# Performance work log

Hardware: AMD Instinct MI355X
Metric: run time of the kernel (lower is better)

Reference implementation:

```python
import jax, jax.numpy as jnp
import numpy as np

N_NODES = 50000
N_EDGES = 800000
N_FEAT = 128
HIDDEN = 64
EMBED = 300
N_CLASSES = 10
N_GRAPHS = 500
LEAKY_SLOPE = 0.01  # torch F.leaky_relu default


def gcn_conv(x, W, b, src, dst, n_nodes):
    # PyG GCNConv: h = x @ W; add self-loops; norm = deg^{-1/2}[src] * deg^{-1/2}[dst]
    h = x @ W  # [N, H]
    deg = jax.ops.segment_sum(jnp.ones_like(dst, dtype=h.dtype), dst, num_segments=n_nodes) + 1.0  # +1 self-loop
    dis = jax.lax.rsqrt(deg)  # deg^{-1/2}, deg >= 1 so finite
    norm = dis[src] * dis[dst]  # [E]
    agg = jax.ops.segment_sum(h[src] * norm[:, None], dst, num_segments=n_nodes)
    agg = agg + h * (dis * dis)[:, None]  # self-loop contribution
    return agg + b


def segment_softmax(s, seg, num_segments):
    # s: [N, 1]; softmax over nodes within each graph
    m = jax.ops.segment_max(s, seg, num_segments=num_segments)
    e = jnp.exp(s - m[seg])
    z = jax.ops.segment_sum(e, seg, num_segments=num_segments)
    return e / z[seg]


def setup_inputs() -> dict:
    key = jax.random.key(0)
    ks = jax.random.split(key, 16)

    def glorot(k, shape):
        fan_in, fan_out = shape[0], shape[1]
        lim = np.sqrt(6.0 / (fan_in + fan_out)).astype(np.float32)
        return jax.random.uniform(k, shape, jnp.float32, -lim, lim)

    x = jax.random.normal(ks[0], (N_NODES, N_FEAT), jnp.float32)
    edge_index = jax.random.randint(ks[1], (2, N_EDGES), 0, N_NODES, dtype=jnp.int64)
    batch = jnp.sort(jax.random.randint(ks[2], (N_NODES,), 0, N_GRAPHS, dtype=jnp.int64))
    return {
        "x": x,
        "edge_index": edge_index,
        "batch": batch,
        "W1": glorot(ks[3], (N_FEAT, HIDDEN)),
        "b1": jnp.zeros((HIDDEN,), jnp.float32),
        "W2": glorot(ks[4], (HIDDEN, HIDDEN)),
        "b2": jnp.zeros((HIDDEN,), jnp.float32),
        "att_w": glorot(ks[5], (HIDDEN, 1)),
        "att_b": jnp.zeros((1,), jnp.float32),
        "proj_w": glorot(ks[6], (HIDDEN, EMBED)),
        "proj_b": jnp.zeros((EMBED,), jnp.float32),
        "cls_w1": glorot(ks[7], (EMBED, 128)),
        "cls_b1": jnp.zeros((128,), jnp.float32),
        "cls_w2": glorot(ks[8], (128, N_CLASSES)),
        "cls_b2": jnp.zeros((N_CLASSES,), jnp.float32),
    }


def reference(x, edge_index, batch, W1, b1, W2, b2, att_w, att_b, proj_w, proj_b, cls_w1, cls_b1, cls_w2, cls_b2):
    src, dst = edge_index[0], edge_index[1]
    n_nodes = x.shape[0]
    h = jax.nn.relu(gcn_conv(x, W1, b1, src, dst, n_nodes))
    # dropout is identity in eval mode
    h = jax.nn.relu(gcn_conv(h, W2, b2, src, dst, n_nodes))  # [N, H]
    att = jax.nn.leaky_relu(h @ att_w + att_b, negative_slope=LEAKY_SLOPE)  # [N, 1]
    att = segment_softmax(att, batch, N_GRAPHS)
    g = jax.ops.segment_sum(att * h, batch, num_segments=N_GRAPHS)  # [G, H]
    g = g @ proj_w + proj_b  # [G, EMBED]
    out = jax.nn.relu(g @ cls_w1 + cls_b1) @ cls_w2 + cls_b2  # [G, num_classes]
    return out
```

## Files before the change

### kernel.cpp

```cpp
#include <hip/hip_runtime.h>
#include <hip/hip_fp16.h>
#include <math.h>

#define N_NODES   50000
#define N_EDGES   800000
#define N_FEAT    128
#define HIDDEN    64
#define EMBED     300
#define N_CLASSES 10
#define N_GRAPHS  500
#define LEAKY     0.01f
#define SCAN_BLOCKS ((N_NODES + 255) / 256)
#define G1_ROWS   32

typedef __attribute__((ext_vector_type(4))) _Float16 half4f;

__device__ __forceinline__ float pk_w(unsigned p) {
    return __half2float(__ushort_as_half((unsigned short)(p >> 16)));
}

__global__ void k_zero(int* deg, int* gs, int* ge) {
    int i = blockIdx.x * 256 + threadIdx.x;
    if (i < N_NODES) deg[i] = 0;
    if (i < N_GRAPHS) { gs[i] = 0; ge[i] = 0; }
}

__global__ void k_deg_rank(const int* __restrict__ dst, int* deg, int* rank) {
    int e = blockIdx.x * 256 + threadIdx.x;
    if (e < N_EDGES) rank[e] = atomicAdd(&deg[dst[e]], 1);
}

__global__ __launch_bounds__(256) void k_scan1(const int* __restrict__ deg, int* row_start,
                                               int* partials, float* dis) {
    __shared__ int wsum[4];
    int i = blockIdx.x * 256 + threadIdx.x;
    int v = (i < N_NODES) ? deg[i] : 0;
    int lane = threadIdx.x & 63, wid = threadIdx.x >> 6;
    int s = v;
    #pragma unroll
    for (int off = 1; off < 64; off <<= 1) {
        int t = __shfl_up(s, off, 64);
        if (lane >= off) s += t;
    }
    if (lane == 63) wsum[wid] = s;
    __syncthreads();
    int woff = 0;
    for (int w = 0; w < wid; ++w) woff += wsum[w];
    if (i < N_NODES) {
        row_start[i] = woff + s - v;
        dis[i] = rsqrtf((float)(deg[i] + 1));
    }
    if (threadIdx.x == 255) partials[blockIdx.x] = woff + s;
}

__global__ __launch_bounds__(256) void k_scan2(int* partials) {
    __shared__ int wsum[4];
    int v = (threadIdx.x < SCAN_BLOCKS) ? partials[threadIdx.x] : 0;
    int lane = threadIdx.x & 63, wid = threadIdx.x >> 6;
    int s = v;
    #pragma unroll
    for (int off = 1; off < 64; off <<= 1) {
        int t = __shfl_up(s, off, 64);
        if (lane >= off) s += t;
    }
    if (lane == 63) wsum[wid] = s;
    __syncthreads();
    int woff = 0;
    for (int w = 0; w < wid; ++w) woff += wsum[w];
    if (threadIdx.x < SCAN_BLOCKS) partials[threadIdx.x] = woff + s - v;
}

__global__ void k_scan3(int* row_start, const int* __restrict__ partials) {
    int i = blockIdx.x * 256 + threadIdx.x;
    if (i < N_NODES) row_start[i] += partials[blockIdx.x];
    if (i == 0) row_start[N_NODES] = N_EDGES;
}

__global__ void k_fill(const int* __restrict__ src, const int* __restrict__ dst,
                       const int* __restrict__ rank, const int* __restrict__ row_start,
                       const float* __restrict__ dis, unsigned* __restrict__ pk) {
    int e = blockIdx.x * 256 + threadIdx.x;
    if (e < N_EDGES) {
        int s = src[e], d = dst[e];
        float w = dis[s] * dis[d];
        unsigned short wh = __half_as_ushort(__float2half(w));
        pk[row_start[d] + rank[e]] = (unsigned)s | ((unsigned)wh << 16);
    }
}

__global__ __launch_bounds__(256) void k_gemm1(const float* __restrict__ x,
                                               const float* __restrict__ W,
                                               __half* __restrict__ h) {
    __shared__ float sW[N_FEAT * HIDDEN];
    __shared__ float sx[G1_ROWS * N_FEAT];
    {
        const float4* W4 = (const float4*)W;
        float4* sW4 = (float4*)sW;
        #pragma unroll
        for (int i = 0; i < N_FEAT * HIDDEN / 4 / 256; ++i)
            sW4[i * 256 + threadIdx.x] = W4[i * 256 + threadIdx.x];

        int base = blockIdx.x * G1_ROWS;
        const float4* x4 = (const float4*)(x + (size_t)base * N_FEAT);
        float4* sx4 = (float4*)sx;
        int lim = (N_NODES - base) * (N_FEAT / 4);
        #pragma unroll
        for (int i = 0; i < G1_ROWS * N_FEAT / 4 / 256; ++i) {
            int idx = i * 256 + threadIdx.x;
            sx4[idx] = (idx < lim) ? x4[idx] : make_float4(0.f, 0.f, 0.f, 0.f);
        }
    }
    __syncthreads();

    int f = threadIdx.x & 63, wid = threadIdx.x >> 6;
    float acc[8];
    #pragma unroll
    for (int u = 0; u < 8; ++u) acc[u] = 0.0f;

    const float4* sx4 = (const float4*)sx;
    #pragma unroll 4
    for (int k4 = 0; k4 < N_FEAT / 4; ++k4) {
        float w0 = sW[(k4 * 4 + 0) * HIDDEN + f];
        float w1 = sW[(k4 * 4 + 1) * HIDDEN + f];
        float w2 = sW[(k4 * 4 + 2) * HIDDEN + f];
        float w3 = sW[(k4 * 4 + 3) * HIDDEN + f];
        #pragma unroll
        for (int u = 0; u < 8; ++u) {
            float4 xv = sx4[(wid * 8 + u) * (N_FEAT / 4) + k4];
            acc[u] = fmaf(xv.x, w0, fmaf(xv.y, w1, fmaf(xv.z, w2, fmaf(xv.w, w3, acc[u]))));
        }
    }
    int base = blockIdx.x * G1_ROWS;
    #pragma unroll
    for (int u = 0; u < 8; ++u) {
        int n = base + wid * 8 + u;
        if (n < N_NODES) h[(size_t)n * HIDDEN + f] = __float2half(acc[u]);
    }
}

__device__ __forceinline__ void gather4pk(const __half* __restrict__ h,
                                          const unsigned* __restrict__ pk,
                                          int s, int e, int lane, int g4, int q,
                                          float4& acc) {
    for (int cs = s; cs < e; cs += 64) {
        unsigned pkv = (cs + lane < e) ? pk[cs + lane] : 0u;
        int avail = e - cs; if (avail > 64) avail = 64;
        int iters = (avail + 3) >> 2;
        #pragma unroll 2
        for (int t = 0; t < iters; ++t) {
            unsigned p = __shfl(pkv, t * 4 + g4, 64);
            float w = pk_w(p);
            half4f hv = *(const half4f*)(h + ((size_t)(p & 0xFFFFu)) * HIDDEN + (q << 2));
            acc.x = fmaf(w, (float)hv.x, acc.x);
            acc.y = fmaf(w, (float)hv.y, acc.y);
            acc.z = fmaf(w, (float)hv.z, acc.z);
            acc.w = fmaf(w, (float)hv.w, acc.w);
        }
    }
}

__device__ __forceinline__ void xreduce(float4& a) {
    a.x += __shfl_xor(a.x, 16, 64); a.y += __shfl_xor(a.y, 16, 64);
    a.z += __shfl_xor(a.z, 16, 64); a.w += __shfl_xor(a.w, 16, 64);
    a.x += __shfl_xor(a.x, 32, 64); a.y += __shfl_xor(a.y, 32, 64);
    a.z += __shfl_xor(a.z, 32, 64); a.w += __shfl_xor(a.w, 32, 64);
}

__global__ __launch_bounds__(256) void k_gg(const __half* __restrict__ h1,
                                            const unsigned* __restrict__ pk,
                                            const int* __restrict__ row_start,
                                            const float* __restrict__ dis,
                                            const float* __restrict__ b1,
                                            const float* __restrict__ W2,
                                            __half* __restrict__ h2) {
    __shared__ float sW[HIDDEN * HIDDEN];
    __shared__ float sa[16 * HIDDEN];
    {
        const float4* W4 = (const float4*)W2;
        float4* sW4 = (float4*)sW;
        #pragma unroll
        for (int i = 0; i < 4; ++i)
            sW4[i * 256 + threadIdx.x] = W4[i * 256 + threadIdx.x];
    }

    int tid = threadIdx.x, wid = tid >> 6, lane = tid & 63;
    int g4 = lane >> 4, q = lane & 15;
    int base = blockIdx.x * 16 + wid * 4;
    #pragma unroll
    for (int i = 0; i < 4; ++i) {
        int node = base + i;
        int s = row_start[node], e = row_start[node + 1];
        float4 acc = {0.f, 0.f, 0.f, 0.f};
        gather4pk(h1, pk, s, e, lane, g4, q, acc);
        xreduce(acc);
        float dv = dis[node], dd = dv * dv;
        half4f sv = *(const half4f*)(h1 + (size_t)node * HIDDEN + (q << 2));
        float4 bv = *(const float4*)(b1 + (q << 2));
        float4 r;
        r.x = fmaxf(fmaf((float)sv.x, dd, bv.x) + acc.x, 0.f);
        r.y = fmaxf(fmaf((float)sv.y, dd, bv.y) + acc.y, 0.f);
        r.z = fmaxf(fmaf((float)sv.z, dd, bv.z) + acc.z, 0.f);
        r.w = fmaxf(fmaf((float)sv.w, dd, bv.w) + acc.w, 0.f);
        if (g4 == 0) *(float4*)&sa[(wid * 4 + i) * HIDDEN + (q << 2)] = r;
    }
    __syncthreads();

    int f = lane;
    float o0 = 0.f, o1 = 0.f, o2 = 0.f, o3 = 0.f;
    const float* sa0 = &sa[wid * 4 * HIDDEN];
    #pragma unroll 8
    for (int k = 0; k < HIDDEN; ++k) {
        float wv = sW[k * HIDDEN + f];
        o0 = fmaf(sa0[k], wv, o0);
        o1 = fmaf(sa0[HIDDEN + k], wv, o1);
        o2 = fmaf(sa0[2 * HIDDEN + k], wv, o2);
        o3 = fmaf(sa0[3 * HIDDEN + k], wv, o3);
    }
    h2[(size_t)(base + 0) * HIDDEN + f] = __float2half(o0);
    h2[(size_t)(base + 1) * HIDDEN + f] = __float2half(o1);
    h2[(size_t)(base + 2) * HIDDEN + f] = __float2half(o2);
    h2[(size_t)(base + 3) * HIDDEN + f] = __float2half(o3);
}

__global__ __launch_bounds__(256) void k_gather2(const __half* __restrict__ h2,
                                                 const unsigned* __restrict__ pk,
                                                 const int* __restrict__ row_start,
                                                 const float* __restrict__ dis,
                                                 const float* __restrict__ b2,
                                                 const float* __restrict__ att_w,
                                                 const float* __restrict__ att_b,
                                                 float* __restrict__ agg2,
                                                 float* __restrict__ att_s) {
    int tid = threadIdx.x, wid = tid >> 6, lane = tid & 63;
    int g4 = lane >> 4, q = lane & 15;
    int node = blockIdx.x * 4 + wid;
    int s = row_start[node], e = row_start[node + 1];
    float4 acc = {0.f, 0.f, 0.f, 0.f};
    gather4pk(h2, pk, s, e, lane, g4, q, acc);
    xreduce(acc);
    float dv = dis[node], dd = dv * dv;
    half4f sv = *(const half4f*)(h2 + (size_t)node * HIDDEN + (q << 2));
    float4 bv = *(const float4*)(b2 + (q << 2));
    float4 r;
    r.x = fmaxf(fmaf((float)sv.x, dd, bv.x) + acc.x, 0.f);
    r.y = fmaxf(fmaf((float)sv.y, dd, bv.y) + acc.y, 0.f);
    r.z = fmaxf(fmaf((float)sv.z, dd, bv.z) + acc.z, 0.f);
    r.w = fmaxf(fmaf((float)sv.w, dd, bv.w) + acc.w, 0.f);
    if (g4 == 0) *(float4*)(agg2 + (size_t)node * HIDDEN + (q << 2)) = r;

    float4 aw = *(const float4*)(att_w + (q << 2));
    float v = fmaf(r.x, aw.x, fmaf(r.y, aw.y, fmaf(r.z, aw.z, r.w * aw.w)));
    v += __shfl_xor(v, 1, 64); v += __shfl_xor(v, 2, 64);
    v += __shfl_xor(v, 4, 64); v += __shfl_xor(v, 8, 64);
    if (lane == 0) {
        float sc = v + att_b[0];
        att_s[node] = (sc > 0.0f) ? sc : LEAKY * sc;
    }
}

__global__ void k_gbounds(const int* __restrict__ batch, int* gs, int* ge) {
    int n = blockIdx.x * 256 + threadIdx.x;
    if (n < N_NODES) {
        int b = batch[n];
        if (n == 0 || batch[n - 1] != b) gs[b] = n;
        if (n == N_NODES - 1 || batch[n + 1] != b) ge[b] = n + 1;
    }
}

__global__ __launch_bounds__(256) void k_pool_head(const float* __restrict__ agg2,
                                                   const float* __restrict__ att_s,
                                                   const int* __restrict__ gs,
                                                   const int* __restrict__ ge,
                                                   const float* __restrict__ proj_w,
                                                   const float* __restrict__ proj_b,
                                                   const float* __restrict__ cls_w1,
                                                   const float* __restrict__ cls_b1,
                                                   const float* __restrict__ cls_w2,
                                                   const float* __restrict__ cls_b2,
                                                   float* __restrict__ out) {
    __shared__ float red[4];
    __shared__ float red2[4 * 64];
    __shared__ float sG[HIDDEN];
    __shared__ float sT1[EMBED];
    __shared__ float sT2[128];
    int gid = blockIdx.x;
    int tid = threadIdx.x, f = tid & 63, w = tid >> 6;
    int s = gs[gid], e = ge[gid];

    float m = -INFINITY;
    for (int n = s + tid; n < e; n += 256) m = fmaxf(m, att_s[n]);
    #pragma unroll
    for (int o = 32; o > 0; o >>= 1) m = fmaxf(m, __shfl_xor(m, o, 64));
    if (f == 0) red[w] = m;
    __syncthreads();
    m = fmaxf(fmaxf(red[0], red[1]), fmaxf(red[2], red[3]));
    __syncthreads();

    float z = 0.0f;
    for (int n = s + tid; n < e; n += 256) z += expf(att_s[n] - m);
    #pragma unroll
    for (int o = 32; o > 0; o >>= 1) z += __shfl_xor(z, o, 64);
    if (f == 0) red[w] = z;
    __syncthreads();
    z = red[0] + red[1] + red[2] + red[3];
    float inv = (e > s) ? 1.0f / z : 0.0f;

    float acc = 0.0f;
    for (int n = s + w; n < e; n += 4)
        acc = fmaf(expf(att_s[n] - m) * inv, agg2[(size_t)n * HIDDEN + f], acc);
    red2[w * 64 + f] = acc;
    __syncthreads();
    if (w == 0) sG[f] = red2[f] + red2[64 + f] + red2[128 + f] + red2[192 + f];
    __syncthreads();

    for (int c = tid; c < EMBED; c += 256) {
        float a = proj_b[c];
        #pragma unroll 8
        for (int k = 0; k < HIDDEN; ++k) a = fmaf(sG[k], proj_w[k * EMBED + c], a);
        sT1[c] = a;
    }
    __syncthreads();

    if (tid < 128) {
        float a = cls_b1[tid];
        for (int k = 0; k < EMBED; ++k) a = fmaf(sT1[k], cls_w1[k * 128 + tid], a);
        sT2[tid] = fmaxf(a, 0.f);
    }
    __syncthreads();

    if (tid < N_CLASSES) {
        float a = cls_b2[tid];
        #pragma unroll 8
        for (int k = 0; k < 128; ++k) a = fmaf(sT2[k], cls_w2[k * N_CLASSES + tid], a);
        out[gid * N_CLASSES + tid] = a;
    }
}

extern "C" void kernel_launch(void* const* d_in, const int* in_sizes, int n_in,
                              void* d_out, int out_size, void* d_ws, size_t ws_size,
                              hipStream_t stream) {
    const float* x      = (const float*)d_in[0];
    const int*   ei     = (const int*)d_in[1];
    const int*   batch  = (const int*)d_in[2];
    const float* W1     = (const float*)d_in[3];
    const float* b1     = (const float*)d_in[4];
    const float* W2     = (const float*)d_in[5];
    const float* b2     = (const float*)d_in[6];
    const float* att_w  = (const float*)d_in[7];
    const float* att_b  = (const float*)d_in[8];
    const float* proj_w = (const float*)d_in[9];
    const float* proj_b = (const float*)d_in[10];
    const float* cls_w1 = (const float*)d_in[11];
    const float* cls_b1 = (const float*)d_in[12];
    const float* cls_w2 = (const float*)d_in[13];
    const float* cls_b2 = (const float*)d_in[14];
    float* out = (float*)d_out;

    const int* e_src = ei;
    const int* e_dst = ei + N_EDGES;

    float* base = (float*)d_ws;
    size_t o = 0;
    float*    dis       = base + o;              o += 50048;
    int*      deg_i     = (int*)(base + o);      o += 50048;
    int*      row_start = (int*)(base + o);      o += 50056;
    int*      partials  = (int*)(base + o);      o += 256;
    unsigned* pk        = (unsigned*)(base + o); o += 800000;
    __half*   h1        = (__half*)(base + o);   o += 1600000;
    __half*   h2        = (__half*)(base + o);   o += 1600000;
    float*    agg2      = base + o;              o += 3200000;
    int*      rank      = (int*)agg2;
    float*    att_s     = base + o;              o += 50048;
    int*      gs        = (int*)(base + o);      o += 512;
    int*      ge        = (int*)(base + o);      o += 512;

    const int NB_N    = (N_NODES + 255) / 256;
    const int NB_E    = (N_EDGES + 255) / 256;
    const int NB_GG   = N_NODES / 16;
    const int NB_ROW4 = N_NODES / 4;
    const int NB_G32  = (N_NODES + G1_ROWS - 1) / G1_ROWS;

    k_zero<<<NB_N, 256, 0, stream>>>(deg_i, gs, ge);
    k_deg_rank<<<NB_E, 256, 0, stream>>>(e_dst, deg_i, rank);
    k_scan1<<<SCAN_BLOCKS, 256, 0, stream>>>(deg_i, row_start, partials, dis);
    k_scan2<<<1, 256, 0, stream>>>(partials);
    k_scan3<<<SCAN_BLOCKS, 256, 0, stream>>>(row_start, partials);
    k_fill<<<NB_E, 256, 0, stream>>>(e_src, e_dst, rank, row_start, dis, pk);

    k_gemm1<<<NB_G32, 256, 0, stream>>>(x, W1, h1);
    k_gg<<<NB_GG, 256, 0, stream>>>(h1, pk, row_start, dis, b1, W2, h2);

    k_gather2<<<NB_ROW4, 256, 0, stream>>>(h2, pk, row_start, dis, b2, att_w, att_b,
                                           agg2, att_s);

    k_gbounds<<<NB_N, 256, 0, stream>>>(batch, gs, ge);
    k_pool_head<<<N_GRAPHS, 256, 0, stream>>>(agg2, att_s, gs, ge,
                                              proj_w, proj_b, cls_w1, cls_b1,
                                              cls_w2, cls_b2, out);
}
```

Before: 193.5 us.

## Compute first GCN projection with fp16 MFMA instead of fp32 FMA

Replaces the shared-memory fp32 FMA GEMM for x@W1 with a wave-level MFMA 16x16x32 f16 kernel. Each wave loads x rows straight from global memory into registers, converts them to half, and multiplies against a transposed fp16 copy of W1 that a new small kernel builds. The aim is to cut the compute and LDS traffic of the first GEMM. In exchange it adds an extra launch and rounds x and W1 to fp16 before the multiply, which adds precision error.

After: 177.1 us. 8.5% less time.

```diff
diff --git a/kernel.cpp b/kernel.cpp
--- a/kernel.cpp
+++ b/kernel.cpp
@@ -11,9 +11,10 @@
 #define N_GRAPHS  500
 #define LEAKY     0.01f
 #define SCAN_BLOCKS ((N_NODES + 255) / 256)
-#define G1_ROWS   32
 
 typedef __attribute__((ext_vector_type(4))) _Float16 half4f;
+typedef __attribute__((ext_vector_type(8))) _Float16 half8;
+typedef __attribute__((ext_vector_type(4))) float f32x4;
 
 __device__ __forceinline__ float pk_w(unsigned p) {
     return __half2float(__ushort_as_half((unsigned short)(p >> 16)));
@@ -23,6 +24,14 @@
     int i = blockIdx.x * 256 + threadIdx.x;
     if (i < N_NODES) deg[i] = 0;
     if (i < N_GRAPHS) { gs[i] = 0; ge[i] = 0; }
+}
+
+__global__ void k_w1t(const float* __restrict__ W1, __half* __restrict__ W1T) {
+    int idx = blockIdx.x * 256 + threadIdx.x;
+    if (idx < N_FEAT * HIDDEN) {
+        int n = idx >> 7, k = idx & 127;
+        W1T[idx] = __float2half(W1[k * HIDDEN + n]);
+    }
 }
 
 __global__ void k_deg_rank(const int* __restrict__ dst, int* deg, int* rank) {
@@ -89,52 +98,42 @@
 }
 
 __global__ __launch_bounds__(256) void k_gemm1(const float* __restrict__ x,
-                                               const float* __restrict__ W,
+                                               const __half* __restrict__ W1T,
                                                __half* __restrict__ h) {
-    __shared__ float sW[N_FEAT * HIDDEN];
-    __shared__ float sx[G1_ROWS * N_FEAT];
-    {
-        const float4* W4 = (const float4*)W;
-        float4* sW4 = (float4*)sW;
+    int tid = threadIdx.x, wid = tid >> 6, lane = tid & 63;
+    int r16 = lane & 15, kg = lane >> 4;
+    int rowbase = blockIdx.x * 64 + wid * 16;
+    int arow = rowbase + r16;
+    bool avalid = arow < N_NODES;
+    const float* xr = x + (size_t)arow * N_FEAT;
+
+    half8 a[4];
+    #pragma unroll
+    for (int kt = 0; kt < 4; ++kt) {
+        int k0 = kt * 32 + kg * 8;
+        float4 u = avalid ? *(const float4*)(xr + k0)     : make_float4(0.f, 0.f, 0.f, 0.f);
+        float4 v = avalid ? *(const float4*)(xr + k0 + 4) : make_float4(0.f, 0.f, 0.f, 0.f);
+        a[kt][0] = (_Float16)u.x; a[kt][1] = (_Float16)u.y;
+        a[kt][2] = (_Float16)u.z; a[kt][3] = (_Float16)u.w;
+        a[kt][4] = (_Float16)v.x; a[kt][5] = (_Float16)v.y;
+        a[kt][6] = (_Float16)v.z; a[kt][7] = (_Float16)v.w;
+    }
+
+    #pragma unroll
+    for (int nt = 0; nt < 4; ++nt) {
+        f32x4 acc = {0.f, 0.f, 0.f, 0.f};
+        const _Float16* wp = (const _Float16*)W1T + (size_t)(nt * 16 + r16) * N_FEAT + kg * 8;
         #pragma unroll
-        for (int i = 0; i < N_FEAT * HIDDEN / 4 / 256; ++i)
-            sW4[i * 256 + threadIdx.x] = W4[i * 256 + threadIdx.x];
-
-        int base = blockIdx.x * G1_ROWS;
-        const float4* x4 = (const float4*)(x + (size_t)base * N_FEAT);
-        float4* sx4 = (float4*)sx;
-        int lim = (N_NODES - base) * (N_FEAT / 4);
+        for (int kt = 0; kt < 4; ++kt) {
+            half8 b = *(const half8*)(wp + kt * 32);
+            acc = __builtin_amdgcn_mfma_f32_16x16x32_f16(a[kt], b, acc, 0, 0, 0);
+        }
+        int col = nt * 16 + r16;
         #pragma unroll
-        for (int i = 0; i < G1_ROWS * N_FEAT / 4 / 256; ++i) {
-            int idx = i * 256 + threadIdx.x;
-            sx4[idx] = (idx < lim) ? x4[idx] : make_float4(0.f, 0.f, 0.f, 0.f);
+        for (int r = 0; r < 4; ++r) {
+            int row = rowbase + kg * 4 + r;
+            if (row < N_NODES) h[(size_t)row * HIDDEN + col] = __float2half(acc[r]);
         }
-    }
-    __syncthreads();
-
-    int f = threadIdx.x & 63, wid = threadIdx.x >> 6;
-    float acc[8];
-    #pragma unroll
-    for (int u = 0; u < 8; ++u) acc[u] = 0.0f;
-
-    const float4* sx4 = (const float4*)sx;
-    #pragma unroll 4
-    for (int k4 = 0; k4 < N_FEAT / 4; ++k4) {
-        float w0 = sW[(k4 * 4 + 0) * HIDDEN + f];
-        float w1 = sW[(k4 * 4 + 1) * HIDDEN + f];
-        float w2 = sW[(k4 * 4 + 2) * HIDDEN + f];
-        float w3 = sW[(k4 * 4 + 3) * HIDDEN + f];
-        #pragma unroll
-        for (int u = 0; u < 8; ++u) {
-            float4 xv = sx4[(wid * 8 + u) * (N_FEAT / 4) + k4];
-            acc[u] = fmaf(xv.x, w0, fmaf(xv.y, w1, fmaf(xv.z, w2, fmaf(xv.w, w3, acc[u]))));
-        }
-    }
-    int base = blockIdx.x * G1_ROWS;
-    #pragma unroll
-    for (int u = 0; u < 8; ++u) {
-        int n = base + wid * 8 + u;
-        if (n < N_NODES) h[(size_t)n * HIDDEN + f] = __float2half(acc[u]);
     }
 }
 
@@ -363,7 +362,7 @@
     size_t o = 0;
     float*    dis       = base + o;              o += 50048;
     int*      deg_i     = (int*)(base + o);      o += 50048;
-    int*      row_start = (int*)(base + o);      o += 50056;
+    int*      row_start = (int*)(base + o);      o += 50080;
     int*      partials  = (int*)(base + o);      o += 256;
     unsigned* pk        = (unsigned*)(base + o); o += 800000;
     __half*   h1        = (__half*)(base + o);   o += 1600000;
@@ -373,21 +372,23 @@
     float*    att_s     = base + o;              o += 50048;
     int*      gs        = (int*)(base + o);      o += 512;
     int*      ge        = (int*)(base + o);      o += 512;
+    __half*   W1T       = (__half*)(base + o);   o += 4096;
 
     const int NB_N    = (N_NODES + 255) / 256;
     const int NB_E    = (N_EDGES + 255) / 256;
     const int NB_GG   = N_NODES / 16;
     const int NB_ROW4 = N_NODES / 4;
-    const int NB_G32  = (N_NODES + G1_ROWS - 1) / G1_ROWS;
+    const int NB_M64  = (N_NODES + 63) / 64;
 
     k_zero<<<NB_N, 256, 0, stream>>>(deg_i, gs, ge);
+    k_w1t<<<(N_FEAT * HIDDEN + 255) / 256, 256, 0, stream>>>(W1, W1T);
     k_deg_rank<<<NB_E, 256, 0, stream>>>(e_dst, deg_i, rank);
     k_scan1<<<SCAN_BLOCKS, 256, 0, stream>>>(deg_i, row_start, partials, dis);
     k_scan2<<<1, 256, 0, stream>>>(partials);
     k_scan3<<<SCAN_BLOCKS, 256, 0, stream>>>(row_start, partials);
     k_fill<<<NB_E, 256, 0, stream>>>(e_src, e_dst, rank, row_start, dis, pk);
 
-    k_gemm1<<<NB_G32, 256, 0, stream>>>(x, W1, h1);
+    k_gemm1<<<NB_M64, 256, 0, stream>>>(x, W1T, h1);
     k_gg<<<NB_GG, 256, 0, stream>>>(h1, pk, row_start, dis, b1, W2, h2);
 
     k_gather2<<<NB_ROW4, 256, 0, stream>>>(h2, pk, row_start, dis, b2, att_w, att_b,
```
